# Optimization experiments

Hardware: AMD Instinct MI355X
Metric: run time of the kernel (lower is better)

The kernel has to match this reference:

```python
import jax, jax.numpy as jnp
import numpy as np

B, T, C, H = 4, 2048, 1024, 16
D = C // H  # head dim = 64

def setup_inputs() -> dict:
    key = jax.random.key(0)
    k1, k2, k3, k4, k5 = jax.random.split(key, 5)
    s_in = 1.0 / np.sqrt(C)
    return {
        "inputs": jax.random.normal(k1, (B, T, C), dtype=jnp.float32),
        "W_qkv": jax.random.normal(k2, (C, 3 * C), dtype=jnp.float32) * s_in,
        "b_qkv": jnp.zeros((3 * C,), dtype=jnp.float32),
        "W_proj": jax.random.normal(k3, (C, C), dtype=jnp.float32) * s_in,
        "b_proj": jnp.zeros((C,), dtype=jnp.float32),
    }

def reference(inputs, W_qkv, b_qkv, W_proj, b_proj):
    Bq, Tq, Cq = inputs.shape
    qkv = inputs @ W_qkv + b_qkv                      # [B,T,3C]
    q, k, v = jnp.split(qkv, 3, axis=-1)              # each [B,T,C]
    # [B,T,C] -> [B,H,T,D]
    def heads(x):
        return x.reshape(Bq, Tq, H, D).transpose(0, 2, 1, 3)
    q, k, v = heads(q), heads(k), heads(v)
    scale = 1.0 / np.sqrt(D)
    att = jnp.einsum('bhqd,bhkd->bhqk', q, k) * scale  # [B,H,T,T]
    causal = jnp.tril(jnp.ones((Tq, Tq), dtype=bool))
    att = jnp.where(causal, att, -jnp.inf)
    att = jax.nn.softmax(att, axis=-1)
    out = jnp.einsum('bhqk,bhkd->bhqd', att, v)        # [B,H,T,D]
    out = out.transpose(0, 2, 1, 3).reshape(Bq, Tq, Cq)
    return out @ W_proj + b_proj
```

## Files before the change

kernel.cpp:

```cpp
#include <hip/hip_runtime.h>

typedef unsigned short u16;
typedef unsigned int u32;
typedef __attribute__((ext_vector_type(8))) short short8;
typedef __attribute__((ext_vector_type(4))) float f32x4;
typedef __attribute__((ext_vector_type(4))) float float4v;
typedef __attribute__((ext_vector_type(4))) unsigned short u16x4;
typedef __attribute__((ext_vector_type(2))) u32 u32x2;

#define DEV __device__ __forceinline__

#define QSCALE 0.18033688011112042f

DEV u16 f2bf(float f) {
  u32 u = __float_as_uint(f);
  u32 r = (u + 0x7fffu + ((u >> 16) & 1u)) >> 16;
  return (u16)r;
}

DEV u32 cvtpk(float lo, float hi) {
  u32 r;
  asm("v_cvt_pk_bf16_f32 %0, %1, %2" : "=v"(r) : "v"(lo), "v"(hi));
  return r;
}

DEV f32x4 mfma16(short8 a, short8 b, f32x4 c) {
  return __builtin_amdgcn_mfma_f32_16x16x32_bf16(a, b, c, 0, 0, 0);
}

DEV void gld_lds16(const void* g, void* l) {
  __builtin_amdgcn_global_load_lds(
      (const __attribute__((address_space(1))) void*)g,
      (__attribute__((address_space(3))) void*)l, 16, 0, 0);
}

__global__ void cvt_x_kernel(const float4v* __restrict__ in,
                             u32x2* __restrict__ out, int n4) {
  int i = blockIdx.x * blockDim.x + threadIdx.x;
  if (i >= n4) return;
  float4v v = in[i];
  u32x2 o;
  o.x = cvtpk(v.x, v.y);
  o.y = cvtpk(v.z, v.w);
  out[i] = o;
}

__global__ void cvt_w_t_kernel(const float* __restrict__ in,
                               u16* __restrict__ out, int Kd, int Nd) {
  __shared__ float tile[32][33];
  int n0 = blockIdx.x * 32, k0 = blockIdx.y * 32;
  int tx = threadIdx.x, ty = threadIdx.y;
#pragma unroll
  for (int j = 0; j < 4; ++j)
    tile[ty + 8 * j][tx] = in[(size_t)(k0 + ty + 8 * j) * Nd + n0 + tx];
  __syncthreads();
#pragma unroll
  for (int j = 0; j < 4; ++j)
    out[(size_t)(n0 + ty + 8 * j) * Kd + k0 + tx] = f2bf(tile[tx][ty + 8 * j]);
}

template <int MODE>
__global__ __launch_bounds__(256, 2) void gemm_bt(
    const u16* __restrict__ A, const u16* __restrict__ Bt,
    const float* __restrict__ bias, u16* __restrict__ q_out,
    u16* __restrict__ k_out, u16* __restrict__ vt_out,
    float* __restrict__ f_out, int M, int N, int K) {
  __shared__ u16 ldsA[128 * 64];
  __shared__ u16 ldsB[128 * 64];
  const int tid = threadIdx.x;
  const int lane = tid & 63, w = tid >> 6;
  const int g = lane >> 4, c = lane & 15;
  const int wm = w >> 1, wn = w & 1;

  const int total = gridDim.x;
  const int cpx = total >> 3;
  const int wg = blockIdx.x;
  const int swz = (wg & 7) * cpx + (wg >> 3);
  const int mtiles = M >> 7;
  const int by = swz & (mtiles - 1);
  const int bx = swz / mtiles;
  const int n0 = bx * 128, m0 = by * 128;

  const f32x4 fz = {0.f, 0.f, 0.f, 0.f};
  f32x4 acc[4][4];
#pragma unroll
  for (int i = 0; i < 4; ++i)
#pragma unroll
    for (int j = 0; j < 4; ++j) acc[i][j] = fz;

  const u16* Ag = A + (size_t)m0 * K;
  const u16* Bg = Bt + (size_t)n0 * K;
  const int lr = lane >> 3;
  const int kc = (lane & 7) ^ lr;

  for (int kt = 0; kt < K; kt += 64) {
#pragma unroll
    for (int qq = 0; qq < 4; ++qq) {
      int row = w * 32 + qq * 8 + lr;
      gld_lds16(Ag + (size_t)row * K + kt + kc * 8, &ldsA[(w * 32 + qq * 8) * 64]);
      gld_lds16(Bg + (size_t)row * K + kt + kc * 8, &ldsB[(w * 32 + qq * 8) * 64]);
    }
    __syncthreads();
#pragma unroll
    for (int ks = 0; ks < 2; ++ks) {
      short8 ar[4], br[4];
#pragma unroll
      for (int mr = 0; mr < 4; ++mr) {
        int row = wm * 64 + mr * 16 + c;
        ar[mr] = *(const short8*)&ldsA[row * 64 + (((ks * 4 + g) ^ (row & 7)) << 3)];
      }
#pragma unroll
      for (int nf = 0; nf < 4; ++nf) {
        int row = wn * 64 + nf * 16 + c;
        br[nf] = *(const short8*)&ldsB[row * 64 + (((ks * 4 + g) ^ (row & 7)) << 3)];
      }
#pragma unroll
      for (int mr = 0; mr < 4; ++mr)
#pragma unroll
        for (int nf = 0; nf < 4; ++nf)
          acc[mr][nf] = mfma16(ar[mr], br[nf], acc[mr][nf]);
    }
    __syncthreads();
  }

#pragma unroll
  for (int mr = 0; mr < 4; ++mr) {
#pragma unroll
    for (int nf = 0; nf < 4; ++nf) {
      const int gm0 = m0 + wm * 64 + mr * 16 + 4 * g;
      const int gn = n0 + wn * 64 + nf * 16 + c;
      float v4[4];
#pragma unroll
      for (int r = 0; r < 4; ++r) v4[r] = acc[mr][nf][r] + bias[gn];
      if (MODE == 0) {
        const int sec = gn >> 10, cc = gn & 1023;
        const int hh = cc >> 6, dd = cc & 63;
        const int bb = gm0 >> 11, tt0 = gm0 & 2047;
        if (sec == 0) {
#pragma unroll
          for (int r = 0; r < 4; ++r)
            q_out[((size_t)(bb * 16 + hh) * 2048 + tt0 + r) * 64 + dd] =
                f2bf(v4[r] * QSCALE);
        } else if (sec == 1) {
#pragma unroll
          for (int r = 0; r < 4; ++r)
            k_out[((size_t)(bb * 16 + hh) * 2048 + tt0 + r) * 64 + dd] =
                f2bf(v4[r]);
        } else {
          u32x2 pkd;
          pkd.x = cvtpk(v4[0], v4[1]);
          pkd.y = cvtpk(v4[2], v4[3]);
          *(u32x2*)&vt_out[((size_t)(bb * 16 + hh) * 64 + dd) * 2048 + tt0] = pkd;
        }
      } else {
#pragma unroll
        for (int r = 0; r < 4; ++r)
          f_out[(size_t)(gm0 + r) * N + gn] = v4[r];
      }
    }
  }
}

__global__ __launch_bounds__(512, 8) void attn_fwd(
    const u16* __restrict__ Qb, const u16* __restrict__ Kb,
    const u16* __restrict__ VTb, u16* __restrict__ Ob) {
  __shared__ u16 lds[2][8192];
  const int lane = threadIdx.x & 63, w = threadIdx.x >> 6;
  const int g = lane >> 4, c = lane & 15;
  const int bi = blockIdx.x;
  const int bh = ((bi & 7) << 3) | ((bi >> 3) & 7);
  const int qblock = 15 - (bi >> 6);
  const int b = bh >> 4, h = bh & 15;
  const size_t base = (size_t)bh * (2048 * 64);
  const u16* Qp = Qb + base;
  const u16* Kp = Kb + base;
  const u16* VTp = VTb + base;

  const int qw = qblock * 128 + w * 16;
  const int qg = qw + c;
  const int nt = 2 * qblock + 2;
  const int tmask = qw >> 6;

  short8 qf0 = *(const short8*)&Qp[(qw + c) * 64 + g * 8];
  short8 qf1 = *(const short8*)&Qp[(qw + c) * 64 + 32 + g * 8];

  const f32x4 fz = {0.f, 0.f, 0.f, 0.f};
  f32x4 o[4];
#pragma unroll
  for (int d0 = 0; d0 < 4; ++d0) o[d0] = fz;
  float m = -1e30f, lsum = 0.f;

  const int srow = lane >> 3;
  const int sgx = (lane & 7) ^ (srow & 7);
  auto stage = [&](int t, int buf) {
#pragma unroll
    for (int q = 0; q < 2; ++q) {
      const int i = w * 2 + q;
      const int row = ((i & 7) << 3) | srow;
      const int k0 = t << 6;
      const u16* src = (i < 8)
          ? Kp + (size_t)(k0 + row) * 64 + sgx * 8
          : VTp + (size_t)row * 2048 + k0 + sgx * 8;
      gld_lds16(src, &lds[buf][i * 512]);
    }
  };

  stage(0, 0);
  __syncthreads();

  for (int t = 0; t < nt; ++t) {
    const int cur = t & 1;
    if (t + 1 < nt) stage(t + 1, cur ^ 1);
    if (t <= tmask) {
      const u16* Kl = &lds[cur][0];
      const u16* Vl = &lds[cur][4096];
      const int k0b = t << 6;
      const int cx = c & 7;

      float pv[16];
      __builtin_amdgcn_s_setprio(1);
#pragma unroll
      for (int j = 0; j < 4; ++j) {
        short8 ka = *(const short8*)&Kl[(16 * j + c) * 64 + ((g ^ cx) << 3)];
        short8 kb = *(const short8*)&Kl[(16 * j + c) * 64 + (((4 + g) ^ cx) << 3)];
        f32x4 s = mfma16(ka, qf0, fz);
        s = mfma16(kb, qf1, s);
#pragma unroll
        for (int r = 0; r < 4; ++r) pv[j * 4 + r] = s[r];
      }
      __builtin_amdgcn_s_setprio(0);

      if (t == tmask) {
#pragma unroll
        for (int j = 0; j < 4; ++j)
#pragma unroll
          for (int r = 0; r < 4; ++r)
            if (k0b + 16 * j + 4 * g + r > qg) pv[j * 4 + r] = -1e30f;
      }

      float mx[8];
#pragma unroll
      for (int i = 0; i < 8; ++i) mx[i] = fmaxf(pv[2 * i], pv[2 * i + 1]);
#pragma unroll
      for (int i = 0; i < 4; ++i) mx[i] = fmaxf(mx[i], mx[i + 4]);
      float tm = fmaxf(fmaxf(mx[0], mx[1]), fmaxf(mx[2], mx[3]));
      tm = fmaxf(tm, __shfl_xor(tm, 16));
      tm = fmaxf(tm, __shfl_xor(tm, 32));

      if (__any(tm > m + 8.f)) {
        float mn = fmaxf(m, tm);
        float sc = __builtin_amdgcn_exp2f(m - mn);
        m = mn;
        lsum *= sc;
#pragma unroll
        for (int d0 = 0; d0 < 4; ++d0)
#pragma unroll
          for (int r = 0; r < 4; ++r) o[d0][r] *= sc;
      }

#pragma unroll
      for (int i = 0; i < 16; ++i) pv[i] = __builtin_amdgcn_exp2f(pv[i] - m);
      float sx[8];
#pragma unroll
      for (int i = 0; i < 8; ++i) sx[i] = pv[2 * i] + pv[2 * i + 1];
#pragma unroll
      for (int i = 0; i < 4; ++i) sx[i] = sx[i] + sx[i + 4];
      float rs = (sx[0] + sx[1]) + (sx[2] + sx[3]);
      rs += __shfl_xor(rs, 16);
      rs += __shfl_xor(rs, 32);
      lsum += rs;

      u32 P2[8];
#pragma unroll
      for (int j = 0; j < 4; ++j) {
        P2[j * 2 + 0] = cvtpk(pv[j * 4 + 0], pv[j * 4 + 1]);
        P2[j * 2 + 1] = cvtpk(pv[j * 4 + 2], pv[j * 4 + 3]);
      }

#pragma unroll
      for (int hh = 0; hh < 2; ++hh) {
        u32 pbw[4];
#pragma unroll
        for (int i = 0; i < 4; ++i) {
          int src = c + ((2 * (g & 1) + (i >> 1)) << 4);
          int a0 = __shfl((int)P2[(2 * hh) * 2 + (i & 1)], src);
          int a1 = __shfl((int)P2[(2 * hh + 1) * 2 + (i & 1)], src);
          pbw[i] = (g < 2) ? (u32)a0 : (u32)a1;
        }
        short8 pb = *(short8*)pbw;
        __builtin_amdgcn_s_setprio(1);
#pragma unroll
        for (int d0 = 0; d0 < 4; ++d0) {
          short8 va = *(const short8*)
              &Vl[(d0 * 16 + c) * 64 + (((4 * hh + g) ^ cx) << 3)];
          o[d0] = mfma16(va, pb, o[d0]);
        }
        __builtin_amdgcn_s_setprio(0);
      }
    }
    __syncthreads();
  }

  float inv = 1.f / lsum;
  u16* Op = Ob + (size_t)(b * 2048 + qw + c) * 1024 + h * 64;
#pragma unroll
  for (int d0 = 0; d0 < 4; ++d0) {
    u32x2 pk;
    pk.x = cvtpk(o[d0][0] * inv, o[d0][1] * inv);
    pk.y = cvtpk(o[d0][2] * inv, o[d0][3] * inv);
    *(u32x2*)(Op + d0 * 16 + 4 * g) = pk;
  }
}

extern "C" void kernel_launch(void* const* d_in, const int* in_sizes, int n_in,
                              void* d_out, int out_size, void* d_ws,
                              size_t ws_size, hipStream_t stream) {
  (void)in_sizes; (void)n_in; (void)out_size; (void)ws_size;
  const float* X = (const float*)d_in[0];
  const float* Wqkv = (const float*)d_in[1];
  const float* bqkv = (const float*)d_in[2];
  const float* Wproj = (const float*)d_in[3];
  const float* bproj = (const float*)d_in[4];
  float* out = (float*)d_out;

  char* ws = (char*)d_ws;
  u16* Xb = (u16*)ws;
  u16* WqkvT = (u16*)(ws + (16u << 20));
  u16* WprojT = (u16*)(ws + (22u << 20));
  u16* Qb = (u16*)(ws + (24u << 20));
  u16* Kb = (u16*)(ws + (40u << 20));
  u16* VT = (u16*)(ws + (56u << 20));

  cvt_x_kernel<<<dim3(8192), dim3(256), 0, stream>>>(
      (const float4v*)X, (u32x2*)Xb, 8192 * 1024 / 4);
  cvt_w_t_kernel<<<dim3(96, 32), dim3(32, 8), 0, stream>>>(Wqkv, WqkvT, 1024, 3072);
  cvt_w_t_kernel<<<dim3(32, 32), dim3(32, 8), 0, stream>>>(Wproj, WprojT, 1024, 1024);

  gemm_bt<0><<<dim3(1536), dim3(256), 0, stream>>>(
      Xb, WqkvT, bqkv, Qb, Kb, VT, (float*)nullptr, 8192, 3072, 1024);

  attn_fwd<<<dim3(1024), dim3(512), 0, stream>>>(Qb, Kb, VT, Xb);

  gemm_bt<1><<<dim3(512), dim3(256), 0, stream>>>(
      Xb, WprojT, bproj, (u16*)nullptr, (u16*)nullptr, (u16*)nullptr, out,
      8192, 1024, 1024);
}
```

Before: 288.8 us.

## Switch attention to 32x32x16 MFMA with 32-query waves and 256-thread blocks

```diff
diff --git a/kernel.cpp b/kernel.cpp
--- a/kernel.cpp
+++ b/kernel.cpp
@@ -4,6 +4,7 @@
 typedef unsigned int u32;
 typedef __attribute__((ext_vector_type(8))) short short8;
 typedef __attribute__((ext_vector_type(4))) float f32x4;
+typedef __attribute__((ext_vector_type(16))) float f32x16;
 typedef __attribute__((ext_vector_type(4))) float float4v;
 typedef __attribute__((ext_vector_type(4))) unsigned short u16x4;
 typedef __attribute__((ext_vector_type(2))) u32 u32x2;
@@ -26,6 +27,10 @@
 
 DEV f32x4 mfma16(short8 a, short8 b, f32x4 c) {
   return __builtin_amdgcn_mfma_f32_16x16x32_bf16(a, b, c, 0, 0, 0);
+}
+
+DEV f32x16 mfma32(short8 a, short8 b, f32x16 c) {
+  return __builtin_amdgcn_mfma_f32_32x32x16_bf16(a, b, c, 0, 0, 0);
 }
 
 DEV void gld_lds16(const void* g, void* l) {
@@ -161,41 +166,44 @@
   }
 }
 
-__global__ __launch_bounds__(512, 8) void attn_fwd(
+__global__ __launch_bounds__(256, 3) void attn_fwd(
     const u16* __restrict__ Qb, const u16* __restrict__ Kb,
     const u16* __restrict__ VTb, u16* __restrict__ Ob) {
   __shared__ u16 lds[2][8192];
   const int lane = threadIdx.x & 63, w = threadIdx.x >> 6;
-  const int g = lane >> 4, c = lane & 15;
+  const int h = lane >> 5;
+  const int q5 = lane & 31;
+  const int l7 = lane & 7;
   const int bi = blockIdx.x;
   const int bh = ((bi & 7) << 3) | ((bi >> 3) & 7);
   const int qblock = 15 - (bi >> 6);
-  const int b = bh >> 4, h = bh & 15;
+  const int b = bh >> 4, hd = bh & 15;
   const size_t base = (size_t)bh * (2048 * 64);
   const u16* Qp = Qb + base;
   const u16* Kp = Kb + base;
   const u16* VTp = VTb + base;
 
-  const int qw = qblock * 128 + w * 16;
-  const int qg = qw + c;
+  const int qw = qblock * 128 + w * 32;
+  const int qg = qw + q5;
   const int nt = 2 * qblock + 2;
   const int tmask = qw >> 6;
 
-  short8 qf0 = *(const short8*)&Qp[(qw + c) * 64 + g * 8];
-  short8 qf1 = *(const short8*)&Qp[(qw + c) * 64 + 32 + g * 8];
-
-  const f32x4 fz = {0.f, 0.f, 0.f, 0.f};
-  f32x4 o[4];
-#pragma unroll
-  for (int d0 = 0; d0 < 4; ++d0) o[d0] = fz;
+  short8 qf[4];
+#pragma unroll
+  for (int dc = 0; dc < 4; ++dc)
+    qf[dc] = *(const short8*)&Qp[(qw + q5) * 64 + dc * 16 + h * 8];
+
+  const f32x16 z16 = {0.f, 0.f, 0.f, 0.f, 0.f, 0.f, 0.f, 0.f,
+                      0.f, 0.f, 0.f, 0.f, 0.f, 0.f, 0.f, 0.f};
+  f32x16 o0 = z16, o1 = z16;
   float m = -1e30f, lsum = 0.f;
 
   const int srow = lane >> 3;
   const int sgx = (lane & 7) ^ (srow & 7);
   auto stage = [&](int t, int buf) {
 #pragma unroll
-    for (int q = 0; q < 2; ++q) {
-      const int i = w * 2 + q;
+    for (int q = 0; q < 4; ++q) {
+      const int i = w * 4 + q;
       const int row = ((i & 7) << 3) | srow;
       const int k0 = t << 6;
       const u16* src = (i < 8)
@@ -215,36 +223,48 @@
       const u16* Kl = &lds[cur][0];
       const u16* Vl = &lds[cur][4096];
       const int k0b = t << 6;
-      const int cx = c & 7;
-
-      float pv[16];
+      const bool full2 = !(t == tmask && !(qw & 32));
+
+      f32x16 p0 = z16, p1 = z16;
       __builtin_amdgcn_s_setprio(1);
 #pragma unroll
-      for (int j = 0; j < 4; ++j) {
-        short8 ka = *(const short8*)&Kl[(16 * j + c) * 64 + ((g ^ cx) << 3)];
-        short8 kb = *(const short8*)&Kl[(16 * j + c) * 64 + (((4 + g) ^ cx) << 3)];
-        f32x4 s = mfma16(ka, qf0, fz);
-        s = mfma16(kb, qf1, s);
-#pragma unroll
-        for (int r = 0; r < 4; ++r) pv[j * 4 + r] = s[r];
+      for (int dc = 0; dc < 4; ++dc) {
+        short8 kf = *(const short8*)&Kl[q5 * 64 + (((dc * 2 + h) ^ l7) << 3)];
+        p0 = mfma32(kf, qf[dc], p0);
+      }
+      if (full2) {
+#pragma unroll
+        for (int dc = 0; dc < 4; ++dc) {
+          short8 kf =
+              *(const short8*)&Kl[(32 + q5) * 64 + (((dc * 2 + h) ^ l7) << 3)];
+          p1 = mfma32(kf, qf[dc], p1);
+        }
       }
       __builtin_amdgcn_s_setprio(0);
 
       if (t == tmask) {
-#pragma unroll
-        for (int j = 0; j < 4; ++j)
-#pragma unroll
-          for (int r = 0; r < 4; ++r)
-            if (k0b + 16 * j + 4 * g + r > qg) pv[j * 4 + r] = -1e30f;
-      }
-
-      float mx[8];
-#pragma unroll
-      for (int i = 0; i < 8; ++i) mx[i] = fmaxf(pv[2 * i], pv[2 * i + 1]);
-#pragma unroll
-      for (int i = 0; i < 4; ++i) mx[i] = fmaxf(mx[i], mx[i + 4]);
-      float tm = fmaxf(fmaxf(mx[0], mx[1]), fmaxf(mx[2], mx[3]));
-      tm = fmaxf(tm, __shfl_xor(tm, 16));
+        if (qw & 32) {
+#pragma unroll
+          for (int reg = 0; reg < 16; ++reg) {
+            int key = k0b + 32 + (reg & 3) + 8 * (reg >> 2) + 4 * h;
+            if (key > qg) p1[reg] = -1e30f;
+          }
+        } else {
+#pragma unroll
+          for (int reg = 0; reg < 16; ++reg) {
+            int key = k0b + (reg & 3) + 8 * (reg >> 2) + 4 * h;
+            if (key > qg) p0[reg] = -1e30f;
+          }
+        }
+      }
+
+      float tm = p0[0];
+#pragma unroll
+      for (int reg = 1; reg < 16; ++reg) tm = fmaxf(tm, p0[reg]);
+      if (full2) {
+#pragma unroll
+        for (int reg = 0; reg < 16; ++reg) tm = fmaxf(tm, p1[reg]);
+      }
       tm = fmaxf(tm, __shfl_xor(tm, 32));
 
       if (__any(tm > m + 8.f)) {
@@ -253,48 +273,61 @@
         m = mn;
         lsum *= sc;
 #pragma unroll
-        for (int d0 = 0; d0 < 4; ++d0)
-#pragma unroll
-          for (int r = 0; r < 4; ++r) o[d0][r] *= sc;
-      }
-
-#pragma unroll
-      for (int i = 0; i < 16; ++i) pv[i] = __builtin_amdgcn_exp2f(pv[i] - m);
-      float sx[8];
-#pragma unroll
-      for (int i = 0; i < 8; ++i) sx[i] = pv[2 * i] + pv[2 * i + 1];
-#pragma unroll
-      for (int i = 0; i < 4; ++i) sx[i] = sx[i] + sx[i + 4];
-      float rs = (sx[0] + sx[1]) + (sx[2] + sx[3]);
-      rs += __shfl_xor(rs, 16);
+        for (int reg = 0; reg < 16; ++reg) {
+          o0[reg] *= sc;
+          o1[reg] *= sc;
+        }
+      }
+
+      float rs = 0.f;
+#pragma unroll
+      for (int reg = 0; reg < 16; ++reg) {
+        p0[reg] = __builtin_amdgcn_exp2f(p0[reg] - m);
+        rs += p0[reg];
+      }
+      if (full2) {
+#pragma unroll
+        for (int reg = 0; reg < 16; ++reg) {
+          p1[reg] = __builtin_amdgcn_exp2f(p1[reg] - m);
+          rs += p1[reg];
+        }
+      }
       rs += __shfl_xor(rs, 32);
       lsum += rs;
 
-      u32 P2[8];
-#pragma unroll
-      for (int j = 0; j < 4; ++j) {
-        P2[j * 2 + 0] = cvtpk(pv[j * 4 + 0], pv[j * 4 + 1]);
-        P2[j * 2 + 1] = cvtpk(pv[j * 4 + 2], pv[j * 4 + 3]);
-      }
-
-#pragma unroll
-      for (int hh = 0; hh < 2; ++hh) {
-        u32 pbw[4];
-#pragma unroll
-        for (int i = 0; i < 4; ++i) {
-          int src = c + ((2 * (g & 1) + (i >> 1)) << 4);
-          int a0 = __shfl((int)P2[(2 * hh) * 2 + (i & 1)], src);
-          int a1 = __shfl((int)P2[(2 * hh + 1) * 2 + (i & 1)], src);
-          pbw[i] = (g < 2) ? (u32)a0 : (u32)a1;
-        }
-        short8 pb = *(short8*)pbw;
+      u32 W2lo[8], W2hi[8];
+#pragma unroll
+      for (int r2 = 0; r2 < 4; ++r2) {
+        W2lo[r2] = cvtpk(p0[4 * r2 + 0], p0[4 * r2 + 1]);
+        W2hi[r2] = cvtpk(p0[4 * r2 + 2], p0[4 * r2 + 3]);
+      }
+      if (full2) {
+#pragma unroll
+        for (int r2 = 0; r2 < 4; ++r2) {
+          W2lo[4 + r2] = cvtpk(p1[4 * r2 + 0], p1[4 * r2 + 1]);
+          W2hi[4 + r2] = cvtpk(p1[4 * r2 + 2], p1[4 * r2 + 3]);
+        }
+      }
+
+      const int nkg = full2 ? 4 : 2;
+      for (int kg = 0; kg < nkg; ++kg) {
+        u32 slo = h ? W2lo[2 * kg] : W2lo[2 * kg + 1];
+        u32 shi = h ? W2hi[2 * kg] : W2hi[2 * kg + 1];
+        u32 rlo = (u32)__shfl_xor((int)slo, 32);
+        u32 rhi = (u32)__shfl_xor((int)shi, 32);
+        union { u32 u[4]; short8 s; } pb;
+        pb.u[0] = h ? rlo : W2lo[2 * kg];
+        pb.u[1] = h ? rhi : W2hi[2 * kg];
+        pb.u[2] = h ? W2lo[2 * kg + 1] : rlo;
+        pb.u[3] = h ? W2hi[2 * kg + 1] : rhi;
+
         __builtin_amdgcn_s_setprio(1);
-#pragma unroll
-        for (int d0 = 0; d0 < 4; ++d0) {
-          short8 va = *(const short8*)
-              &Vl[(d0 * 16 + c) * 64 + (((4 * hh + g) ^ cx) << 3)];
-          o[d0] = mfma16(va, pb, o[d0]);
-        }
+        short8 va0 =
+            *(const short8*)&Vl[q5 * 64 + (((kg * 2 + h) ^ l7) << 3)];
+        o0 = mfma32(va0, pb.s, o0);
+        short8 va1 =
+            *(const short8*)&Vl[(32 + q5) * 64 + (((kg * 2 + h) ^ l7) << 3)];
+        o1 = mfma32(va1, pb.s, o1);
         __builtin_amdgcn_s_setprio(0);
       }
     }
@@ -302,13 +335,16 @@
   }
 
   float inv = 1.f / lsum;
-  u16* Op = Ob + (size_t)(b * 2048 + qw + c) * 1024 + h * 64;
-#pragma unroll
-  for (int d0 = 0; d0 < 4; ++d0) {
-    u32x2 pk;
-    pk.x = cvtpk(o[d0][0] * inv, o[d0][1] * inv);
-    pk.y = cvtpk(o[d0][2] * inv, o[d0][3] * inv);
-    *(u32x2*)(Op + d0 * 16 + 4 * g) = pk;
+  u16* Op = Ob + (size_t)(b * 2048 + qw + q5) * 1024 + hd * 64;
+#pragma unroll
+  for (int r2 = 0; r2 < 4; ++r2) {
+    u32x2 pk0, pk1;
+    pk0.x = cvtpk(o0[4 * r2 + 0] * inv, o0[4 * r2 + 1] * inv);
+    pk0.y = cvtpk(o0[4 * r2 + 2] * inv, o0[4 * r2 + 3] * inv);
+    *(u32x2*)(Op + 8 * r2 + 4 * h) = pk0;
+    pk1.x = cvtpk(o1[4 * r2 + 0] * inv, o1[4 * r2 + 1] * inv);
+    pk1.y = cvtpk(o1[4 * r2 + 2] * inv, o1[4 * r2 + 3] * inv);
+    *(u32x2*)(Op + 32 + 8 * r2 + 4 * h) = pk1;
   }
 }
 
@@ -339,7 +375,7 @@
   gemm_bt<0><<<dim3(1536), dim3(256), 0, stream>>>(
       Xb, WqkvT, bqkv, Qb, Kb, VT, (float*)nullptr, 8192, 3072, 1024);
 
-  attn_fwd<<<dim3(1024), dim3(512), 0, stream>>>(Qb, Kb, VT, Xb);
+  attn_fwd<<<dim3(1024), dim3(256), 0, stream>>>(Qb, Kb, VT, Xb);
 
   gemm_bt<1><<<dim3(512), dim3(256), 0, stream>>>(
       Xb, WprojT, bproj, (u16*)nullptr, (u16*)nullptr, (u16*)nullptr, out,
```

New measurement: 303.0 us. +4.9%, slower.
